# Kernel optimization log

Hardware: AMD Instinct MI355X
Metric: run time of the kernel (lower is better)

Reference implementation:

```python
import jax, jax.numpy as jnp
import numpy as np

CH = 256
RED = 4
CQK = CH // RED

def _conv(x, w, b):
    # x: [B,C,H,W], w: [O,I,3,3], b: [O]; SAME padding (pad=1)
    y = jax.lax.conv_general_dilated(
        x, w, window_strides=(1, 1), padding=((1, 1), (1, 1)),
        dimension_numbers=('NCHW', 'OIHW', 'NCHW'))
    return y + b[None, :, None, None]

def setup_inputs() -> dict:
    key = jax.random.key(0)
    ks = jax.random.split(key, 7)
    x = jax.random.normal(ks[0], (4, CH, 64, 64), dtype=jnp.float32)
    fan_in = CH * 9
    s = 1.0 / np.sqrt(fan_in)
    q_w = jax.random.uniform(ks[1], (CQK, CH, 3, 3), jnp.float32, -s, s)
    q_b = jax.random.uniform(ks[2], (CQK,), jnp.float32, -s, s)
    k_w = jax.random.uniform(ks[3], (CQK, CH, 3, 3), jnp.float32, -s, s)
    k_b = jax.random.uniform(ks[4], (CQK,), jnp.float32, -s, s)
    v_w = jax.random.uniform(ks[5], (CH, CH, 3, 3), jnp.float32, -s, s)
    v_b = jax.random.uniform(ks[6], (CH,), jnp.float32, -s, s)
    return {"x": x, "q_w": q_w, "q_b": q_b, "k_w": k_w, "k_b": k_b,
            "v_w": v_w, "v_b": v_b}

def reference(x, q_w, q_b, k_w, k_b, v_w, v_b):
    b, c, h, w = x.shape
    hw = h * w
    scale = CQK ** (-0.5)
    q = _conv(x, q_w, q_b).reshape(b, CQK, hw)   # [B, Cqk, HW]
    k = _conv(x, k_w, k_b).reshape(b, CQK, hw)   # [B, Cqk, HW]
    v = _conv(x, v_w, v_b).reshape(b, c, hw)     # [B, C,   HW]
    # attn[b,i,j] = sum_d q[b,d,i] * k[b,d,j]
    attn = jnp.einsum('bdi,bdj->bij', q, k) * scale
    attn = jax.nn.softmax(attn, axis=-1)         # [B, HW, HW]
    # out[b,c,i] = sum_j v[b,c,j] * attn[b,i,j]  (torch: bmm(v, attn^T))
    out = jnp.einsum('bcj,bij->bci', v, attn).reshape(b, c, h, w)
    return out
```

## Files before the change

kernel.cpp:

```cpp
#include <hip/hip_runtime.h>
#include <stdint.h>

typedef unsigned short u16;
typedef short short8 __attribute__((ext_vector_type(8)));
typedef short short4v __attribute__((ext_vector_type(4)));
typedef float float4v __attribute__((ext_vector_type(4)));
typedef uint32_t uint2v __attribute__((ext_vector_type(2)));

#define HW 4096
#define SCL 0.18033688011112042f

#define GLOAD_LDS(g, l) __builtin_amdgcn_global_load_lds( \
    (const __attribute__((address_space(1))) void*)(g),   \
    (__attribute__((address_space(3))) void*)(l), 16, 0, 0)

static __device__ __forceinline__ u16 f2bf(float f) {
  union { float f; uint32_t u; } v; v.f = f;
  uint32_t r = v.u + 0x7fffu + ((v.u >> 16) & 1u);
  return (u16)(r >> 16);
}
static __device__ __forceinline__ uint32_t f2bf_u32(float f) {
  union { float f; uint32_t u; } v; v.f = f;
  return (v.u + 0x8000u) >> 16;
}

__global__ __launch_bounds__(256) void k_xt(const float* __restrict__ x, u16* __restrict__ Xtp) {
  __shared__ float t[32][33];
  const int b = blockIdx.z, c0 = blockIdx.y * 32, p0 = blockIdx.x * 32;
  const int tid = threadIdx.x;
  const int l8 = tid >> 5, lp = tid & 31;
#pragma unroll
  for (int i = 0; i < 4; i++) {
    int c = l8 + i * 8;
    t[c][lp] = x[(size_t)(b * 256 + c0 + c) * HW + p0 + lp];
  }
  __syncthreads();
#pragma unroll
  for (int i = 0; i < 4; i++) {
    int p = l8 + i * 8;
    int pp = p0 + p;
    int y = pp >> 6, xx = pp & 63;
    Xtp[((size_t)(b * 66 + y + 1) * 66 + (xx + 1)) * 256 + c0 + lp] = f2bf(t[lp][p]);
  }
}

__global__ __launch_bounds__(256) void k_wprep(const float* __restrict__ qw, const float* __restrict__ qb,
    const float* __restrict__ kw, const float* __restrict__ kb,
    const float* __restrict__ vw, const float* __restrict__ vb,
    u16* __restrict__ Wt, float* __restrict__ bcat) {
  int tid = blockIdx.x * 256 + threadIdx.x;
  if (tid < 9 * 384 * 256) {
    int ci = tid & 255;
    int n = (tid >> 8) % 384;
    int off = tid / (384 * 256);
    float val;
    if (n < 64)       val = qw[(size_t)n * 2304 + ci * 9 + off];
    else if (n < 128) val = kw[(size_t)(n - 64) * 2304 + ci * 9 + off];
    else              val = vw[(size_t)(n - 128) * 2304 + ci * 9 + off];
    Wt[tid] = f2bf(val);
  }
  if (tid < 384) bcat[tid] = (tid < 64) ? qb[tid] : (tid < 128) ? kb[tid - 64] : vb[tid - 128];
}

__global__ __launch_bounds__(256) void k_conv(const u16* __restrict__ Xtp,
    const u16* __restrict__ Wt, const float* __restrict__ bcat,
    u16* __restrict__ Qt, u16* __restrict__ Kt, u16* __restrict__ Vcf) {
  __shared__ __align__(16) u16 Als[2][128 * 64];
  __shared__ __align__(16) u16 Bls[2][64 * 64];
  const int tid = threadIdx.x;
  const int b = blockIdx.z, ct = blockIdx.y;
  const int p0 = blockIdx.x * 128, n0 = ct * 64;
  const int w = tid >> 6, lane = tid & 63, l16 = lane & 15, quad = lane >> 4;

  const int lr = lane >> 3, lcx = (lane & 7) ^ lr;
  const u16* ag[4];
#pragma unroll
  for (int g = 0; g < 4; g++) {
    const int pos = p0 + w * 32 + g * 8 + lr;
    const int py = pos >> 6, px = pos & 63;
    ag[g] = Xtp + ((size_t)(b * 66 + py) * 66 + px) * 256 + lcx * 8;
  }
  const u16* bg[2];
#pragma unroll
  for (int g = 0; g < 2; g++)
    bg[g] = Wt + (size_t)(n0 + w * 16 + g * 8 + lr) * 256 + lcx * 8;

  const int rx = l16 & 7;

  float4v acc[2][4];
  const float4v zz = {0.f, 0.f, 0.f, 0.f};
#pragma unroll
  for (int i = 0; i < 2; i++)
#pragma unroll
    for (int j = 0; j < 4; j++) acc[i][j] = zz;

#pragma unroll
  for (int g = 0; g < 4; g++) GLOAD_LDS(ag[g], &Als[0][(w * 32 + g * 8) * 64]);
#pragma unroll
  for (int g = 0; g < 2; g++) GLOAD_LDS(bg[g], &Bls[0][(w * 16 + g * 8) * 64]);
  __syncthreads();

  for (int ks = 0; ks < 36; ks++) {
    const int buf = ks & 1;
    if (ks + 1 < 36) {
      const int ksn = ks + 1, tap = ksn >> 2, cg = (ksn & 3) * 64;
      const int dy = (tap * 11) >> 5, dx = tap - dy * 3;
      const int aoff = (dy * 66 + dx) * 256 + cg;
      const size_t boff = (size_t)tap * 98304 + cg;
#pragma unroll
      for (int g = 0; g < 4; g++) GLOAD_LDS(ag[g] + aoff, &Als[buf ^ 1][(w * 32 + g * 8) * 64]);
#pragma unroll
      for (int g = 0; g < 2; g++) GLOAD_LDS(bg[g] + boff, &Bls[buf ^ 1][(w * 16 + g * 8) * 64]);
    }

    short8 af[2][2], bfv[4][2];
#pragma unroll
    for (int mt = 0; mt < 2; mt++)
#pragma unroll
      for (int kk = 0; kk < 2; kk++)
        af[mt][kk] = *(const short8*)&Als[buf][(w * 32 + mt * 16 + l16) * 64 + (((kk * 4 + quad) ^ rx) * 8)];
#pragma unroll
    for (int nt = 0; nt < 4; nt++)
#pragma unroll
      for (int kk = 0; kk < 2; kk++)
        bfv[nt][kk] = *(const short8*)&Bls[buf][(nt * 16 + l16) * 64 + (((kk * 4 + quad) ^ rx) * 8)];

    if (ct < 2) {
#pragma unroll
      for (int mt = 0; mt < 2; mt++)
#pragma unroll
        for (int nt = 0; nt < 4; nt++)
#pragma unroll
          for (int kk = 0; kk < 2; kk++)
            acc[mt][nt] = __builtin_amdgcn_mfma_f32_16x16x32_bf16(bfv[nt][kk], af[mt][kk], acc[mt][nt], 0, 0, 0);
    } else {
#pragma unroll
      for (int mt = 0; mt < 2; mt++)
#pragma unroll
        for (int nt = 0; nt < 4; nt++)
#pragma unroll
          for (int kk = 0; kk < 2; kk++)
            acc[mt][nt] = __builtin_amdgcn_mfma_f32_16x16x32_bf16(af[mt][kk], bfv[nt][kk], acc[mt][nt], 0, 0, 0);
    }
    __syncthreads();
  }

  if (ct < 2) {
    u16* base = (ct == 0) ? Qt : Kt;
#pragma unroll
    for (int mt = 0; mt < 2; mt++) {
      const int p = p0 + w * 32 + mt * 16 + l16;
#pragma unroll
      for (int nt = 0; nt < 4; nt++) {
        const int nb = nt * 16 + quad * 4;
        short4v o;
#pragma unroll
        for (int r = 0; r < 4; r++) o[r] = (short)f2bf(acc[mt][nt][r] + bcat[ct * 64 + nb + r]);
        *(short4v*)(base + (size_t)(b * HW + p) * 64 + nb) = o;
      }
    }
  } else {
#pragma unroll
    for (int mt = 0; mt < 2; mt++) {
      const int pb = p0 + w * 32 + mt * 16 + quad * 4;
#pragma unroll
      for (int nt = 0; nt < 4; nt++) {
        const int cl = nt * 16 + l16;
        const int gc = (ct - 2) * 64 + cl;
        const float bias = bcat[ct * 64 + cl];
        short4v o;
#pragma unroll
        for (int r = 0; r < 4; r++) o[r] = (short)f2bf(acc[mt][nt][r] + bias);
        *(short4v*)(Vcf + (size_t)(b * 256 + gc) * HW + pb) = o;
      }
    }
  }
}

__global__ __launch_bounds__(256, 2) void k_attn(const u16* __restrict__ Qt,
    const u16* __restrict__ Kt, const u16* __restrict__ Vcf, float* __restrict__ out) {
  __shared__ __align__(16) u16 Kls[2][64 * 64];
  __shared__ __align__(16) u16 Vls[2][128 * 64];
  __shared__ __align__(16) u16 Pls[4][16][66];
  const int tid = threadIdx.x;
  const int b = blockIdx.y, ib = blockIdx.x * 64, cs = blockIdx.z * 128;
  const int w = tid >> 6, lane = tid & 63, l16 = lane & 15, quad = lane >> 4;
  const int i0 = ib + w * 16;

  const u16* Kb = Kt + (size_t)b * HW * 64;
  const u16* Vb = Vcf + ((size_t)b * 256 + cs) * HW;

  const int lr = lane >> 3, lcx = (lane & 7) ^ lr;
  const size_t koff = (size_t)lr * 128 + (size_t)lcx * 16;
  const size_t voff = (size_t)lr * (HW * 2) + (size_t)lcx * 16;

  const int kA = (quad ^ (l16 & 7)) * 8;
  const int rowu = l16 * 64;

  short8 qf[2];
  {
    const u16* qp = Qt + (size_t)(b * HW + i0 + l16) * 64 + quad * 8;
    qf[0] = *(const short8*)qp;
    qf[1] = *(const short8*)(qp + 32);
  }

  float4v of[8];
  const float4v zz = {0.f, 0.f, 0.f, 0.f};
#pragma unroll
  for (int nt = 0; nt < 8; nt++) of[nt] = zz;
  float lsum = 0.f;

  {
    const char* kg = (const char*)Kb + (size_t)(w * 16) * 128;
    const char* vg = (const char*)Vb + (size_t)(w * 32) * (HW * 2);
#pragma unroll
    for (int g = 0; g < 2; g++)
      GLOAD_LDS(kg + g * 1024 + koff, &Kls[0][(w * 16 + g * 8) * 64]);
#pragma unroll
    for (int g = 0; g < 4; g++)
      GLOAD_LDS(vg + (size_t)g * 8 * (HW * 2) + voff, &Vls[0][(w * 32 + g * 8) * 64]);
  }
  __syncthreads();

  for (int jt = 0; jt < 64; jt++) {
    const int buf = jt & 1;
    {
      const int jn = ((jt + 1) & 63) * 64;
      const char* kg = (const char*)Kb + (size_t)(jn + w * 16) * 128;
      const char* vg = (const char*)Vb + (size_t)(w * 32) * (HW * 2) + (size_t)jn * 2;
#pragma unroll
      for (int g = 0; g < 2; g++)
        GLOAD_LDS(kg + g * 1024 + koff, &Kls[buf ^ 1][(w * 16 + g * 8) * 64]);
#pragma unroll
      for (int g = 0; g < 4; g++)
        GLOAD_LDS(vg + (size_t)g * 8 * (HW * 2) + voff, &Vls[buf ^ 1][(w * 32 + g * 8) * 64]);
    }

    float4v sf[4];
#pragma unroll
    for (int nt = 0; nt < 4; nt++) sf[nt] = zz;
#pragma unroll
    for (int nt = 0; nt < 4; nt++) {
      short8 k0 = *(const short8*)&Kls[buf][nt * 1024 + rowu + kA];
      short8 k1 = *(const short8*)&Kls[buf][nt * 1024 + rowu + (kA ^ 32)];
      sf[nt] = __builtin_amdgcn_mfma_f32_16x16x32_bf16(k0, qf[0], sf[nt], 0, 0, 0);
      sf[nt] = __builtin_amdgcn_mfma_f32_16x16x32_bf16(k1, qf[1], sf[nt], 0, 0, 0);
    }

    float rs = 0.f;
#pragma unroll
    for (int nt = 0; nt < 4; nt++) {
      float p0 = exp2f(sf[nt][0] * SCL);
      float p1 = exp2f(sf[nt][1] * SCL);
      float p2 = exp2f(sf[nt][2] * SCL);
      float p3 = exp2f(sf[nt][3] * SCL);
      rs += (p0 + p1) + (p2 + p3);
      uint2v pd;
      pd[0] = f2bf_u32(p0) | (f2bf_u32(p1) << 16);
      pd[1] = f2bf_u32(p2) | (f2bf_u32(p3) << 16);
      *(uint2v*)&Pls[w][l16][nt * 16 + quad * 4] = pd;
    }
    rs += __shfl_xor(rs, 16);
    rs += __shfl_xor(rs, 32);
    lsum += rs;

    __builtin_amdgcn_sched_barrier(0);
    __builtin_amdgcn_s_waitcnt(0xC07F);
    __builtin_amdgcn_sched_barrier(0);

#pragma unroll
    for (int kk = 0; kk < 2; kk++) {
      short8 pfr = *(const short8*)&Pls[w][l16][kk * 32 + quad * 8];
      const int vcol = kk ? (kA ^ 32) : kA;
#pragma unroll
      for (int nt = 0; nt < 8; nt++) {
        short8 vf = *(const short8*)&Vls[buf][nt * 1024 + rowu + vcol];
        of[nt] = __builtin_amdgcn_mfma_f32_16x16x32_bf16(vf, pfr, of[nt], 0, 0, 0);
      }
    }
    __syncthreads();
  }

  const float inv = 1.0f / lsum;
#pragma unroll
  for (int nt = 0; nt < 8; nt++)
#pragma unroll
    for (int r = 0; r < 4; r++)
      out[(size_t)(b * 256 + cs + nt * 16 + quad * 4 + r) * HW + i0 + l16] = of[nt][r] * inv;
}

extern "C" void kernel_launch(void* const* d_in, const int* in_sizes, int n_in,
                              void* d_out, int out_size, void* d_ws, size_t ws_size,
                              hipStream_t stream) {
  const float* x  = (const float*)d_in[0];
  const float* qw = (const float*)d_in[1];
  const float* qb = (const float*)d_in[2];
  const float* kw = (const float*)d_in[3];
  const float* kb = (const float*)d_in[4];
  const float* vw = (const float*)d_in[5];
  const float* vb = (const float*)d_in[6];
  float* out = (float*)d_out;
  char* ws = (char*)d_ws;
  u16*   Xtp = (u16*)(ws);
  u16*   Wt  = (u16*)(ws + 8921088);
  float* bc  = (float*)(ws + 10690560);
  u16*   Qt  = (u16*)(ws + 10692096);
  u16*   Kt  = (u16*)(ws + 12789248);
  u16*   Vcf = (u16*)(ws + 14886400);

  hipMemsetAsync(Xtp, 0, 8921088, stream);
  k_xt  <<<dim3(128, 8, 4), 256, 0, stream>>>(x, Xtp);
  k_wprep<<<3456, 256, 0, stream>>>(qw, qb, kw, kb, vw, vb, Wt, bc);
  k_conv<<<dim3(32, 6, 4), 256, 0, stream>>>(Xtp, Wt, bc, Qt, Kt, Vcf);
  k_attn<<<dim3(64, 4, 2), 256, 0, stream>>>(Qt, Kt, Vcf, out);
}
```

Before: 212.4 us.

## Restructure attention kernel into 512-thread blocks covering all channels with 32x32 MFMA

The attention kernel now uses 512-thread blocks that handle all 256 output channels for a 64-query tile. This removes the old channel split across two blocks, so QK^T and exp are no longer computed twice. Score computation is split across 8 waves (4 key blocks by 2 query halves) and written into a shared swizzled P tile. The PV product then uses 32x32x16 MFMAs, with row sums reduced across waves through LDS. The query scale is folded into Q during the conv epilogue, and bf16 packing switches to the v_cvt_pk_bf16_f32 instruction. The trade-offs are a larger LDS footprint (V tile doubled), a full block barrier every iteration, and higher register pressure.

```diff
diff --git a/kernel.cpp b/kernel.cpp
--- a/kernel.cpp
+++ b/kernel.cpp
@@ -5,10 +5,11 @@
 typedef short short8 __attribute__((ext_vector_type(8)));
 typedef short short4v __attribute__((ext_vector_type(4)));
 typedef float float4v __attribute__((ext_vector_type(4)));
+typedef float float16v __attribute__((ext_vector_type(16)));
 typedef uint32_t uint2v __attribute__((ext_vector_type(2)));
 
 #define HW 4096
-#define SCL 0.18033688011112042f
+#define QSCL 0.18033688011112042f
 
 #define GLOAD_LDS(g, l) __builtin_amdgcn_global_load_lds( \
     (const __attribute__((address_space(1))) void*)(g),   \
@@ -19,9 +20,11 @@
   uint32_t r = v.u + 0x7fffu + ((v.u >> 16) & 1u);
   return (u16)(r >> 16);
 }
-static __device__ __forceinline__ uint32_t f2bf_u32(float f) {
-  union { float f; uint32_t u; } v; v.f = f;
-  return (v.u + 0x8000u) >> 16;
+
+static __device__ __forceinline__ uint32_t pkbf(float a, float b) {
+  uint32_t r;
+  asm("v_cvt_pk_bf16_f32 %0, %1, %2" : "=v"(r) : "v"(a), "v"(b));
+  return r;
 }
 
 __global__ __launch_bounds__(256) void k_xt(const float* __restrict__ x, u16* __restrict__ Xtp) {
@@ -147,6 +150,7 @@
 
   if (ct < 2) {
     u16* base = (ct == 0) ? Qt : Kt;
+    const float qs = (ct == 0) ? QSCL : 1.0f;
 #pragma unroll
     for (int mt = 0; mt < 2; mt++) {
       const int p = p0 + w * 32 + mt * 16 + l16;
@@ -155,7 +159,7 @@
         const int nb = nt * 16 + quad * 4;
         short4v o;
 #pragma unroll
-        for (int r = 0; r < 4; r++) o[r] = (short)f2bf(acc[mt][nt][r] + bcat[ct * 64 + nb + r]);
+        for (int r = 0; r < 4; r++) o[r] = (short)f2bf((acc[mt][nt][r] + bcat[ct * 64 + nb + r]) * qs);
         *(short4v*)(base + (size_t)(b * HW + p) * 64 + nb) = o;
       }
     }
@@ -177,116 +181,129 @@
   }
 }
 
-__global__ __launch_bounds__(256, 2) void k_attn(const u16* __restrict__ Qt,
+__global__ __launch_bounds__(512, 2) void k_attn(const u16* __restrict__ Qt,
     const u16* __restrict__ Kt, const u16* __restrict__ Vcf, float* __restrict__ out) {
   __shared__ __align__(16) u16 Kls[2][64 * 64];
-  __shared__ __align__(16) u16 Vls[2][128 * 64];
-  __shared__ __align__(16) u16 Pls[4][16][66];
+  __shared__ __align__(16) u16 Vls[2][256 * 64];
+  __shared__ __align__(16) u16 Pls[64 * 64];
+  __shared__ float Lls[4][64];
+
   const int tid = threadIdx.x;
-  const int b = blockIdx.y, ib = blockIdx.x * 64, cs = blockIdx.z * 128;
-  const int w = tid >> 6, lane = tid & 63, l16 = lane & 15, quad = lane >> 4;
-  const int i0 = ib + w * 16;
+  const int b = blockIdx.y, ib = blockIdx.x * 64;
+  const int w = tid >> 6, lane = tid & 63;
+  const int l16 = lane & 15, quad = lane >> 4;
+  const int l32 = lane & 31, half = lane >> 5;
+  const int jb = w & 3, ih = w >> 2;
+  const int cb = w;
 
   const u16* Kb = Kt + (size_t)b * HW * 64;
-  const u16* Vb = Vcf + ((size_t)b * 256 + cs) * HW;
+  const u16* Vb = Vcf + (size_t)b * 256 * HW;
 
   const int lr = lane >> 3, lcx = (lane & 7) ^ lr;
-  const size_t koff = (size_t)lr * 128 + (size_t)lcx * 16;
+  const size_t koff = (size_t)(w * 8 + lr) * 128 + (size_t)lcx * 16;
   const size_t voff = (size_t)lr * (HW * 2) + (size_t)lcx * 16;
 
-  const int kA = (quad ^ (l16 & 7)) * 8;
-  const int rowu = l16 * 64;
-
-  short8 qf[2];
+  const int krow = (jb * 16 + l16) * 64;
+  const int kc0 = (quad ^ (l16 & 7)) * 8;
+  const int kc1 = ((4 + quad) ^ (l16 & 7)) * 8;
+
+  short8 qf[2][2];
   {
-    const u16* qp = Qt + (size_t)(b * HW + i0 + l16) * 64 + quad * 8;
-    qf[0] = *(const short8*)qp;
-    qf[1] = *(const short8*)(qp + 32);
-  }
-
-  float4v of[8];
+    const u16* qp = Qt + ((size_t)(b * HW + ib + ih * 32 + l16)) * 64 + quad * 8;
+    qf[0][0] = *(const short8*)qp;
+    qf[0][1] = *(const short8*)(qp + 32);
+    qf[1][0] = *(const short8*)(qp + 16 * 64);
+    qf[1][1] = *(const short8*)(qp + 16 * 64 + 32);
+  }
+
+  const int vrow = (cb * 32 + l32) * 64;
+  const int rx5 = l32 & 7;
+  const int prow0 = l32 * 64, prow1 = (32 + l32) * 64;
+
+  float16v of0, of1;
+#pragma unroll
+  for (int r = 0; r < 16; r++) { of0[r] = 0.f; of1[r] = 0.f; }
+  float lp0 = 0.f, lp1 = 0.f;
   const float4v zz = {0.f, 0.f, 0.f, 0.f};
-#pragma unroll
-  for (int nt = 0; nt < 8; nt++) of[nt] = zz;
-  float lsum = 0.f;
-
-  {
-    const char* kg = (const char*)Kb + (size_t)(w * 16) * 128;
-    const char* vg = (const char*)Vb + (size_t)(w * 32) * (HW * 2);
-#pragma unroll
-    for (int g = 0; g < 2; g++)
-      GLOAD_LDS(kg + g * 1024 + koff, &Kls[0][(w * 16 + g * 8) * 64]);
-#pragma unroll
-    for (int g = 0; g < 4; g++)
-      GLOAD_LDS(vg + (size_t)g * 8 * (HW * 2) + voff, &Vls[0][(w * 32 + g * 8) * 64]);
-  }
+
+  GLOAD_LDS((const char*)Kb + koff, &Kls[0][(w * 8) * 64]);
+#pragma unroll
+  for (int g = 0; g < 4; g++)
+    GLOAD_LDS((const char*)Vb + (size_t)(w * 32 + g * 8) * (HW * 2) + voff,
+              &Vls[0][(w * 32 + g * 8) * 64]);
   __syncthreads();
 
   for (int jt = 0; jt < 64; jt++) {
     const int buf = jt & 1;
     {
       const int jn = ((jt + 1) & 63) * 64;
-      const char* kg = (const char*)Kb + (size_t)(jn + w * 16) * 128;
-      const char* vg = (const char*)Vb + (size_t)(w * 32) * (HW * 2) + (size_t)jn * 2;
-#pragma unroll
-      for (int g = 0; g < 2; g++)
-        GLOAD_LDS(kg + g * 1024 + koff, &Kls[buf ^ 1][(w * 16 + g * 8) * 64]);
+      GLOAD_LDS((const char*)Kb + (size_t)jn * 128 + koff, &Kls[buf ^ 1][(w * 8) * 64]);
 #pragma unroll
       for (int g = 0; g < 4; g++)
-        GLOAD_LDS(vg + (size_t)g * 8 * (HW * 2) + voff, &Vls[buf ^ 1][(w * 32 + g * 8) * 64]);
-    }
-
-    float4v sf[4];
-#pragma unroll
-    for (int nt = 0; nt < 4; nt++) sf[nt] = zz;
-#pragma unroll
-    for (int nt = 0; nt < 4; nt++) {
-      short8 k0 = *(const short8*)&Kls[buf][nt * 1024 + rowu + kA];
-      short8 k1 = *(const short8*)&Kls[buf][nt * 1024 + rowu + (kA ^ 32)];
-      sf[nt] = __builtin_amdgcn_mfma_f32_16x16x32_bf16(k0, qf[0], sf[nt], 0, 0, 0);
-      sf[nt] = __builtin_amdgcn_mfma_f32_16x16x32_bf16(k1, qf[1], sf[nt], 0, 0, 0);
-    }
-
-    float rs = 0.f;
-#pragma unroll
-    for (int nt = 0; nt < 4; nt++) {
-      float p0 = exp2f(sf[nt][0] * SCL);
-      float p1 = exp2f(sf[nt][1] * SCL);
-      float p2 = exp2f(sf[nt][2] * SCL);
-      float p3 = exp2f(sf[nt][3] * SCL);
-      rs += (p0 + p1) + (p2 + p3);
-      uint2v pd;
-      pd[0] = f2bf_u32(p0) | (f2bf_u32(p1) << 16);
-      pd[1] = f2bf_u32(p2) | (f2bf_u32(p3) << 16);
-      *(uint2v*)&Pls[w][l16][nt * 16 + quad * 4] = pd;
-    }
-    rs += __shfl_xor(rs, 16);
-    rs += __shfl_xor(rs, 32);
-    lsum += rs;
+        GLOAD_LDS((const char*)Vb + (size_t)(w * 32 + g * 8) * (HW * 2) + (size_t)jn * 2 + voff,
+                  &Vls[buf ^ 1][(w * 32 + g * 8) * 64]);
+    }
+
+    short8 k0 = *(const short8*)&Kls[buf][krow + kc0];
+    short8 k1 = *(const short8*)&Kls[buf][krow + kc1];
+    float4v s0 = zz, s1 = zz;
+    s0 = __builtin_amdgcn_mfma_f32_16x16x32_bf16(k0, qf[0][0], s0, 0, 0, 0);
+    s0 = __builtin_amdgcn_mfma_f32_16x16x32_bf16(k1, qf[0][1], s0, 0, 0, 0);
+    s1 = __builtin_amdgcn_mfma_f32_16x16x32_bf16(k0, qf[1][0], s1, 0, 0, 0);
+    s1 = __builtin_amdgcn_mfma_f32_16x16x32_bf16(k1, qf[1][1], s1, 0, 0, 0);
+
+    {
+      float p0 = exp2f(s0[0]), p1 = exp2f(s0[1]), p2 = exp2f(s0[2]), p3 = exp2f(s0[3]);
+      lp0 += (p0 + p1) + (p2 + p3);
+      uint2v pd; pd[0] = pkbf(p0, p1); pd[1] = pkbf(p2, p3);
+      const int row = ih * 32 + l16;
+      *(uint2v*)&Pls[row * 64 + (((jb * 2 + (quad >> 1)) ^ (row & 7)) * 8) + (quad & 1) * 4] = pd;
+    }
+    {
+      float p0 = exp2f(s1[0]), p1 = exp2f(s1[1]), p2 = exp2f(s1[2]), p3 = exp2f(s1[3]);
+      lp1 += (p0 + p1) + (p2 + p3);
+      uint2v pd; pd[0] = pkbf(p0, p1); pd[1] = pkbf(p2, p3);
+      const int row = ih * 32 + 16 + l16;
+      *(uint2v*)&Pls[row * 64 + (((jb * 2 + (quad >> 1)) ^ (row & 7)) * 8) + (quad & 1) * 4] = pd;
+    }
 
     __builtin_amdgcn_sched_barrier(0);
-    __builtin_amdgcn_s_waitcnt(0xC07F);
-    __builtin_amdgcn_sched_barrier(0);
-
-#pragma unroll
-    for (int kk = 0; kk < 2; kk++) {
-      short8 pfr = *(const short8*)&Pls[w][l16][kk * 32 + quad * 8];
-      const int vcol = kk ? (kA ^ 32) : kA;
-#pragma unroll
-      for (int nt = 0; nt < 8; nt++) {
-        short8 vf = *(const short8*)&Vls[buf][nt * 1024 + rowu + vcol];
-        of[nt] = __builtin_amdgcn_mfma_f32_16x16x32_bf16(vf, pfr, of[nt], 0, 0, 0);
-      }
-    }
+    asm volatile("s_waitcnt lgkmcnt(0)" ::: "memory");
+    __builtin_amdgcn_s_barrier();
+    asm volatile("" ::: "memory");
+
+    __builtin_amdgcn_s_setprio(1);
+#pragma unroll
+    for (int jk = 0; jk < 4; jk++) {
+      const int ch = jk * 2 + half;
+      short8 vf  = *(const short8*)&Vls[buf][vrow + ((ch ^ rx5) * 8)];
+      short8 pf0 = *(const short8*)&Pls[prow0 + ((ch ^ rx5) * 8)];
+      short8 pf1 = *(const short8*)&Pls[prow1 + ((ch ^ rx5) * 8)];
+      of0 = __builtin_amdgcn_mfma_f32_32x32x16_bf16(vf, pf0, of0, 0, 0, 0);
+      of1 = __builtin_amdgcn_mfma_f32_32x32x16_bf16(vf, pf1, of1, 0, 0, 0);
+    }
+    __builtin_amdgcn_s_setprio(0);
     __syncthreads();
   }
 
-  const float inv = 1.0f / lsum;
-#pragma unroll
-  for (int nt = 0; nt < 8; nt++)
-#pragma unroll
-    for (int r = 0; r < 4; r++)
-      out[(size_t)(b * 256 + cs + nt * 16 + quad * 4 + r) * HW + i0 + l16] = of[nt][r] * inv;
+  lp0 += __shfl_xor(lp0, 16); lp0 += __shfl_xor(lp0, 32);
+  lp1 += __shfl_xor(lp1, 16); lp1 += __shfl_xor(lp1, 32);
+  if (quad == 0) {
+    Lls[jb][ih * 32 + l16] = lp0;
+    Lls[jb][ih * 32 + 16 + l16] = lp1;
+  }
+  __syncthreads();
+
+#pragma unroll
+  for (int it = 0; it < 2; it++) {
+    const int ii = it * 32 + l32;
+    const float inv = 1.0f / ((Lls[0][ii] + Lls[1][ii]) + (Lls[2][ii] + Lls[3][ii]));
+    float* ob = out + (size_t)(b * 256 + cb * 32 + 4 * half) * HW + ib + ii;
+    const float16v o = it ? of1 : of0;
+#pragma unroll
+    for (int r = 0; r < 16; r++)
+      ob[(size_t)((r & 3) + 8 * (r >> 2)) * HW] = o[r] * inv;
+  }
 }
 
 extern "C" void kernel_launch(void* const* d_in, const int* in_sizes, int n_in,
@@ -312,5 +329,5 @@
   k_xt  <<<dim3(128, 8, 4), 256, 0, stream>>>(x, Xtp);
   k_wprep<<<3456, 256, 0, stream>>>(qw, qb, kw, kb, vw, vb, Wt, bc);
   k_conv<<<dim3(32, 6, 4), 256, 0, stream>>>(Xtp, Wt, bc, Qt, Kt, Vcf);
-  k_attn<<<dim3(64, 4, 2), 256, 0, stream>>>(Qt, Kt, Vcf, out);
-}
+  k_attn<<<dim3(64, 4), 512, 0, stream>>>(Qt, Kt, Vcf, out);
+}
```

Result: no change. 211.8 us (-0.3%).
